# Kernel tuning notes

Measured on AMD Instinct MI355X. Metric: run time of the kernel, lower is better.

## Reference

```python
import jax, jax.numpy as jnp
import numpy as np

HEAD_NUM = 16

def setup_inputs() -> dict:
    key = jax.random.key(0)
    kq, kk, kv = jax.random.split(key, 3)
    shape = (4, 2048, 1024)  # [B, N, C]
    return {
        "query_layer": jax.random.normal(kq, shape, dtype=jnp.float32),
        "key_layer": jax.random.normal(kk, shape, dtype=jnp.float32),
        "value_layer": jax.random.normal(kv, shape, dtype=jnp.float32),
    }

def _split_heads(x, h):
    B, N, C = x.shape
    return x.reshape(B, N, h, C // h).transpose(0, 2, 1, 3)  # [B,H,N,d]

def reference(query_layer, key_layer, value_layer):
    B, N, C = query_layer.shape
    h = HEAD_NUM
    d = C // h
    q = _split_heads(query_layer, h)
    k = _split_heads(key_layer, h)
    v = _split_heads(value_layer, h)
    scores = jnp.einsum('bhnd,bhmd->bhnm', q, k) / jnp.sqrt(jnp.asarray(d, q.dtype))
    probs = jax.nn.softmax(scores, axis=-1)
    ctx = jnp.einsum('bhnm,bhmd->bhnd', probs, v)
    return ctx.transpose(0, 2, 1, 3).reshape(B, N, C)
```

## Files before the change

kernel.cpp:

```cpp
#include <hip/hip_runtime.h>
#include <hip/hip_bf16.h>

#define B_   4
#define N_   2048
#define C_   1024
#define NT   32
#define QSCALE 0.18033688011112042f

typedef __attribute__((ext_vector_type(8)))  short short8;
typedef __attribute__((ext_vector_type(4)))  float f32x4;
typedef __attribute__((ext_vector_type(16))) float f32x16;
typedef __attribute__((ext_vector_type(2)))  int   int2v;

__device__ __forceinline__ unsigned short f2bf(float x) {
    union { __hip_bfloat16 h; unsigned short u; } c;
    c.h = __float2bfloat16(x);
    return c.u;
}
__device__ __forceinline__ float fast_exp2(float x) {
    float r; asm("v_exp_f32 %0, %1" : "=v"(r) : "v"(x)); return r;
}
__device__ __forceinline__ int cvtpk(float a, float b) {
    int r; asm("v_cvt_pk_bf16_f32 %0, %1, %2" : "=v"(r) : "v"(a), "v"(b)); return r;
}

__global__ __launch_bounds__(256) void prepack(
    const float* __restrict__ K, const float* __restrict__ V,
    unsigned short* __restrict__ Kt, unsigned short* __restrict__ Vt)
{
    __shared__ __align__(16) unsigned short kl[4096];
    __shared__ __align__(16) unsigned short vl[4096];
    const int L = blockIdx.x;
    const int xcd = L & 7;
    const int j = L >> 3;
    const int head = xcd + 8 * (j >> 5);
    const int t = j & 31;
    const int b = head >> 4, h = head & 15;
    const int tid = threadIdx.x;
    const int r = tid >> 2, cb = tid & 3;
    const size_t head_off = (size_t)b * N_ * C_ + (size_t)h * 64;
    const int kv0 = t * 64;
    const int blk_out = head * NT + t;

    {
        const float* src = K + head_off + (size_t)(kv0 + r) * C_ + cb * 16;
        f32x4 x0 = *(const f32x4*)(src);
        f32x4 x1 = *(const f32x4*)(src + 4);
        f32x4 x2 = *(const f32x4*)(src + 8);
        f32x4 x3 = *(const f32x4*)(src + 12);
        short8 p0, p1;
        #pragma unroll
        for (int i = 0; i < 4; ++i) {
            p0[i] = (short)f2bf(x0[i]); p0[i + 4] = (short)f2bf(x1[i]);
            p1[i] = (short)f2bf(x2[i]); p1[i + 4] = (short)f2bf(x3[i]);
        }
        const int swz = (r & 7) << 3;
        *(short8*)&kl[r * 64 + ((cb * 16) ^ swz)]     = p0;
        *(short8*)&kl[r * 64 + ((cb * 16 + 8) ^ swz)] = p1;
    }
    {
        const float* src = V + head_off + (size_t)(kv0 + r) * C_ + cb * 16;
        f32x4 y0 = *(const f32x4*)(src);
        f32x4 y1 = *(const f32x4*)(src + 4);
        f32x4 y2 = *(const f32x4*)(src + 8);
        f32x4 y3 = *(const f32x4*)(src + 12);
        #pragma unroll
        for (int i = 0; i < 4; ++i) {
            int d0 = cb * 16 + i;
            vl[d0 * 64 + (r ^ ((d0 & 7) << 3))] = f2bf(y0[i]);
            int d1 = cb * 16 + 4 + i;
            vl[d1 * 64 + (r ^ ((d1 & 7) << 3))] = f2bf(y1[i]);
            int d2 = cb * 16 + 8 + i;
            vl[d2 * 64 + (r ^ ((d2 & 7) << 3))] = f2bf(y2[i]);
            int d3 = cb * 16 + 12 + i;
            vl[d3 * 64 + (r ^ ((d3 & 7) << 3))] = f2bf(y3[i]);
        }
    }
    __syncthreads();
    #pragma unroll
    for (int cc = 0; cc < 2; ++cc) {
        const int c  = tid + cc * 256;
        const int f  = c >> 6;
        const int ln = c & 63;
        const int row = (f & 1) * 32 + (ln & 31);
        const int col = (f >> 1) * 16 + (ln >> 5) * 8;
        const int sw  = (row & 7) << 3;
        short8 kk = *(const short8*)&kl[row * 64 + (col ^ sw)];
        short8 vv = *(const short8*)&vl[row * 64 + (col ^ sw)];
        *(short8*)&Kt[(size_t)blk_out * 4096 + c * 8] = kk;
        *(short8*)&Vt[(size_t)blk_out * 4096 + c * 8] = vv;
    }
}

__global__ __launch_bounds__(256, 4) void attn_fwd(
    const float* __restrict__ Q, const unsigned short* __restrict__ Kt,
    const unsigned short* __restrict__ Vt, float* __restrict__ O)
{
    const int L = blockIdx.x;
    const int xcd = L & 7;
    const int j = L >> 3;
    const int head = xcd + 8 * (j >> 4);
    const int qt = j & 15;
    const int b = head >> 4, h = head & 15;

    const int tid  = threadIdx.x;
    const int wave = tid >> 6;
    const int lane = tid & 63;
    const int l31  = lane & 31;
    const int hi   = lane >> 5;

    const unsigned short* kbase = Kt + (size_t)head * (NT * 4096);
    const unsigned short* vbase = Vt + (size_t)head * (NT * 4096);
    const float* qp = Q + (size_t)b * N_ * C_ + (size_t)h * 64;
    float*       op = O + (size_t)b * N_ * C_ + (size_t)h * 64;

    const int qrow = qt * 128 + wave * 32 + l31;
    short8 qfrag[4];
    {
        const float* qr = qp + (size_t)qrow * C_ + hi * 8;
        #pragma unroll
        for (int ks = 0; ks < 4; ++ks) {
            f32x4 x0 = *(const f32x4*)(qr + ks * 16);
            f32x4 x1 = *(const f32x4*)(qr + ks * 16 + 4);
            short8 a;
            #pragma unroll
            for (int i = 0; i < 4; ++i) {
                a[i]     = (short)f2bf(x0[i] * QSCALE);
                a[i + 4] = (short)f2bf(x1[i] * QSCALE);
            }
            qfrag[ks] = a;
        }
    }

    f32x16 o0 = {}, o1 = {};
    float m_r = -3.0e38f, l_r = 0.0f;

    const int lofs = lane * 8;

    for (int t = 0; t < NT; ++t) {
        const unsigned short* ktp = kbase + (size_t)t * 4096;
        const unsigned short* vtp = vbase + (size_t)t * 4096;

        f32x16 s0 = {}, s1 = {};
        __builtin_amdgcn_s_setprio(1);
        #pragma unroll
        for (int ks = 0; ks < 4; ++ks) {
            short8 kf0 = *(const short8*)(ktp + ks * 1024 + lofs);
            short8 kf1 = *(const short8*)(ktp + ks * 1024 + 512 + lofs);
            s0 = __builtin_amdgcn_mfma_f32_32x32x16_bf16(kf0, qfrag[ks], s0, 0, 0, 0);
            s1 = __builtin_amdgcn_mfma_f32_32x32x16_bf16(kf1, qfrag[ks], s1, 0, 0, 0);
        }
        __builtin_amdgcn_s_setprio(0);

        float mx[8];
        #pragma unroll
        for (int r = 0; r < 8; ++r) mx[r] = fmaxf(fmaxf(s0[r], s0[r + 8]), fmaxf(s1[r], s1[r + 8]));
        #pragma unroll
        for (int st = 4; st; st >>= 1) {
            #pragma unroll
            for (int r = 0; r < st; ++r) mx[r] = fmaxf(mx[r], mx[r + st]);
        }
        int2v msw = __builtin_amdgcn_permlane32_swap(__float_as_int(mx[0]), __float_as_int(mx[0]), false, false);
        const float rm = fmaxf(__int_as_float(msw[0]), __int_as_float(msw[1]));

        if (!__all(rm - m_r <= 8.0f)) {
            const float mnew = fmaxf(m_r, rm);
            const float corr = fast_exp2(m_r - mnew);
            m_r = mnew;
            l_r *= corr;
            #pragma unroll
            for (int r = 0; r < 16; ++r) { o0[r] *= corr; o1[r] *= corr; }
        }

        #pragma unroll
        for (int r = 0; r < 16; ++r) {
            s0[r] = fast_exp2(s0[r] - m_r);
            s1[r] = fast_exp2(s1[r] - m_r);
        }
        float aa[8];
        #pragma unroll
        for (int r = 0; r < 8; ++r) aa[r] = (s0[r] + s0[r + 8]) + (s1[r] + s1[r + 8]);
        #pragma unroll
        for (int st = 4; st; st >>= 1) {
            #pragma unroll
            for (int r = 0; r < st; ++r) aa[r] += aa[r + st];
        }
        int2v ssw = __builtin_amdgcn_permlane32_swap(__float_as_int(aa[0]), __float_as_int(aa[0]), false, false);
        l_r += __int_as_float(ssw[0]) + __int_as_float(ssw[1]);

        short8 pf[4];
        #pragma unroll
        for (int ct = 0; ct < 2; ++ct) {
            #pragma unroll
            for (int kss = 0; kss < 2; ++kss) {
                float e0, e1, e2, e3, e4, e5, e6, e7;
                if (ct == 0) {
                    e0 = s0[8*kss+0]; e1 = s0[8*kss+1]; e2 = s0[8*kss+2]; e3 = s0[8*kss+3];
                    e4 = s0[8*kss+4]; e5 = s0[8*kss+5]; e6 = s0[8*kss+6]; e7 = s0[8*kss+7];
                } else {
                    e0 = s1[8*kss+0]; e1 = s1[8*kss+1]; e2 = s1[8*kss+2]; e3 = s1[8*kss+3];
                    e4 = s1[8*kss+4]; e5 = s1[8*kss+5]; e6 = s1[8*kss+6]; e7 = s1[8*kss+7];
                }
                int w0 = cvtpk(e0, e1);
                int w1 = cvtpk(e2, e3);
                int w2 = cvtpk(e4, e5);
                int w3 = cvtpk(e6, e7);
                int2v sA = __builtin_amdgcn_permlane32_swap(w0, w2, false, false);
                int2v sB = __builtin_amdgcn_permlane32_swap(w1, w3, false, false);
                union { int i[4]; short8 v; } u;
                u.i[0] = sA[0]; u.i[1] = sB[0]; u.i[2] = sA[1]; u.i[3] = sB[1];
                pf[ct * 2 + kss] = u.v;
            }
        }

        __builtin_amdgcn_s_setprio(1);
        #pragma unroll
        for (int ks = 0; ks < 4; ++ks) {
            short8 vf0 = *(const short8*)(vtp + ks * 1024 + lofs);
            short8 vf1 = *(const short8*)(vtp + ks * 1024 + 512 + lofs);
            o0 = __builtin_amdgcn_mfma_f32_32x32x16_bf16(vf0, pf[ks], o0, 0, 0, 0);
            o1 = __builtin_amdgcn_mfma_f32_32x32x16_bf16(vf1, pf[ks], o1, 0, 0, 0);
        }
        __builtin_amdgcn_s_setprio(0);
    }

    const float inv = 1.0f / l_r;
    float* orow = op + (size_t)qrow * C_;
    #pragma unroll
    for (int bb = 0; bb < 4; ++bb) {
        f32x4 w0, w1;
        #pragma unroll
        for (int i = 0; i < 4; ++i) {
            w0[i] = o0[4 * bb + i] * inv;
            w1[i] = o1[4 * bb + i] * inv;
        }
        *(f32x4*)(orow + 8 * bb + 4 * hi)      = w0;
        *(f32x4*)(orow + 32 + 8 * bb + 4 * hi) = w1;
    }
}

extern "C" void kernel_launch(void* const* d_in, const int* in_sizes, int n_in,
                              void* d_out, int out_size, void* d_ws, size_t ws_size,
                              hipStream_t stream) {
    const float* q = (const float*)d_in[0];
    const float* k = (const float*)d_in[1];
    const float* v = (const float*)d_in[2];
    float* o = (float*)d_out;
    unsigned short* Kt = (unsigned short*)d_ws;
    unsigned short* Vt = Kt + (size_t)64 * NT * 4096;
    prepack<<<dim3(64 * NT), dim3(256), 0, stream>>>(k, v, Kt, Vt);
    attn_fwd<<<dim3(1024), dim3(256), 0, stream>>>(q, Kt, Vt, o);
}
```

Measured before the change: 120.9 us.

## Stage K/V tiles into double-buffered LDS via async global_load_lds

Each wave now asynchronously copies a quarter of the next K and V tile into a double-buffered shared-memory buffer with global_load_lds. The MFMA loops then read fragments from LDS instead of from global memory. This removes the fourfold redundant global reads across waves and overlaps the next tile's fetch with the current compute. In exchange it adds a vmcnt wait and a block barrier every iteration, plus 32KB of LDS per block, which may constrain occupancy.

```diff
diff --git a/kernel.cpp b/kernel.cpp
--- a/kernel.cpp
+++ b/kernel.cpp
@@ -96,6 +96,9 @@
     const float* __restrict__ Q, const unsigned short* __restrict__ Kt,
     const unsigned short* __restrict__ Vt, float* __restrict__ O)
 {
+    __shared__ __align__(16) unsigned short klds[2][4096];
+    __shared__ __align__(16) unsigned short vlds[2][4096];
+
     const int L = blockIdx.x;
     const int xcd = L & 7;
     const int j = L >> 3;
@@ -137,16 +140,36 @@
 
     const int lofs = lane * 8;
 
+    auto stage = [&](int t, int buf) {
+        const unsigned short* kg = kbase + (size_t)t * 4096 + wave * 1024 + lofs;
+        const unsigned short* vg = vbase + (size_t)t * 4096 + wave * 1024 + lofs;
+        __builtin_amdgcn_global_load_lds((const __attribute__((address_space(1))) void*)kg,
+            (__attribute__((address_space(3))) void*)&klds[buf][wave * 1024], 16, 0, 0);
+        __builtin_amdgcn_global_load_lds((const __attribute__((address_space(1))) void*)(kg + 512),
+            (__attribute__((address_space(3))) void*)&klds[buf][wave * 1024 + 512], 16, 0, 0);
+        __builtin_amdgcn_global_load_lds((const __attribute__((address_space(1))) void*)vg,
+            (__attribute__((address_space(3))) void*)&vlds[buf][wave * 1024], 16, 0, 0);
+        __builtin_amdgcn_global_load_lds((const __attribute__((address_space(1))) void*)(vg + 512),
+            (__attribute__((address_space(3))) void*)&vlds[buf][wave * 1024 + 512], 16, 0, 0);
+    };
+
+    stage(0, 0);
+    int cur = 0;
+
     for (int t = 0; t < NT; ++t) {
-        const unsigned short* ktp = kbase + (size_t)t * 4096;
-        const unsigned short* vtp = vbase + (size_t)t * 4096;
+        asm volatile("s_waitcnt vmcnt(0)" ::: "memory");
+        __syncthreads();
+        if (t + 1 < NT) stage(t + 1, cur ^ 1);
+
+        const unsigned short* kl = klds[cur];
+        const unsigned short* vl = vlds[cur];
 
         f32x16 s0 = {}, s1 = {};
         __builtin_amdgcn_s_setprio(1);
         #pragma unroll
         for (int ks = 0; ks < 4; ++ks) {
-            short8 kf0 = *(const short8*)(ktp + ks * 1024 + lofs);
-            short8 kf1 = *(const short8*)(ktp + ks * 1024 + 512 + lofs);
+            short8 kf0 = *(const short8*)&kl[ks * 1024 + lofs];
+            short8 kf1 = *(const short8*)&kl[ks * 1024 + 512 + lofs];
             s0 = __builtin_amdgcn_mfma_f32_32x32x16_bf16(kf0, qfrag[ks], s0, 0, 0, 0);
             s1 = __builtin_amdgcn_mfma_f32_32x32x16_bf16(kf1, qfrag[ks], s1, 0, 0, 0);
         }
@@ -216,12 +239,14 @@
         __builtin_amdgcn_s_setprio(1);
         #pragma unroll
         for (int ks = 0; ks < 4; ++ks) {
-            short8 vf0 = *(const short8*)(vtp + ks * 1024 + lofs);
-            short8 vf1 = *(const short8*)(vtp + ks * 1024 + 512 + lofs);
+            short8 vf0 = *(const short8*)&vl[ks * 1024 + lofs];
+            short8 vf1 = *(const short8*)&vl[ks * 1024 + 512 + lofs];
             o0 = __builtin_amdgcn_mfma_f32_32x32x16_bf16(vf0, pf[ks], o0, 0, 0, 0);
             o1 = __builtin_amdgcn_mfma_f32_32x32x16_bf16(vf1, pf[ks], o1, 0, 0, 0);
         }
         __builtin_amdgcn_s_setprio(0);
+
+        cur ^= 1;
     }
 
     const float inv = 1.0f / l_r;
```

Measured after the change: 111.5 us. -7.8%, faster.

## Software-pipeline attention loop with LDS double-buffered K and deferred PV MFMA

Applied to the files above, without the earlier changes.

Restructures the attention main loop into a software pipeline. K tiles are staged into a double-buffered LDS array via global_load_lds. The PV MFMAs of the previous tile are issued right after the current QK MFMAs, and V fragments for the current tile are prefetched into registers. The running max is folded into the QK accumulator init so the subtraction is skipped, and the row-sum permlane reduction is deferred to the end. This aims to hide global-load latency and softmax VALU work behind MFMAs, at the cost of more registers (occupancy hint lowered from 4 to 3) and a barrier per tile.

```diff
diff --git a/kernel.cpp b/kernel.cpp
--- a/kernel.cpp
+++ b/kernel.cpp
@@ -92,10 +92,135 @@
     }
 }
 
-__global__ __launch_bounds__(256, 4) void attn_fwd(
+#define MFMA32(A, B, C) __builtin_amdgcn_mfma_f32_32x32x16_bf16((A), (B), (C), 0, 0, 0)
+
+#define TILE_BODY(T, PO0, PO1, PO2, PO3, PI0, PI1, PI2, PI3, FIRST)            \
+{                                                                              \
+    asm volatile("s_waitcnt vmcnt(0)" ::: "memory");                           \
+    __syncthreads();                                                           \
+    if ((T) + 1 < NT) stageK((T) + 1, cur ^ 1);                                \
+    const unsigned short* kl = &klds[cur][0];                                  \
+    f32x16 s0, s1;                                                             \
+    {                                                                          \
+        const float nm = (FIRST) ? 0.0f : -m_r;   \
+        _Pragma("unroll")                                                      \
+        for (int r = 0; r < 16; ++r) { s0[r] = nm; s1[r] = nm; }               \
+    }                                                                          \
+    __builtin_amdgcn_s_setprio(1);                                             \
+    {                                                                          \
+        short8 kf0 = *(const short8*)&kl[0 * 1024 + lofs];                     \
+        short8 kf1 = *(const short8*)&kl[0 * 1024 + 512 + lofs];               \
+        s0 = MFMA32(kf0, qfrag[0], s0);                                        \
+        s1 = MFMA32(kf1, qfrag[0], s1);                                        \
+        kf0 = *(const short8*)&kl[1 * 1024 + lofs];                            \
+        kf1 = *(const short8*)&kl[1 * 1024 + 512 + lofs];                      \
+        s0 = MFMA32(kf0, qfrag[1], s0);                                        \
+        s1 = MFMA32(kf1, qfrag[1], s1);                                        \
+        kf0 = *(const short8*)&kl[2 * 1024 + lofs];                            \
+        kf1 = *(const short8*)&kl[2 * 1024 + 512 + lofs];                      \
+        s0 = MFMA32(kf0, qfrag[2], s0);                                        \
+        s1 = MFMA32(kf1, qfrag[2], s1);                                        \
+        kf0 = *(const short8*)&kl[3 * 1024 + lofs];                            \
+        kf1 = *(const short8*)&kl[3 * 1024 + 512 + lofs];                      \
+        s0 = MFMA32(kf0, qfrag[3], s0);                                        \
+        s1 = MFMA32(kf1, qfrag[3], s1);                                        \
+    }                                                                          \
+    if (!(FIRST)) {      \
+        o0 = MFMA32(vr0, PI0, o0);  o1 = MFMA32(vr1, PI0, o1);                 \
+        o0 = MFMA32(vr2, PI1, o0);  o1 = MFMA32(vr3, PI1, o1);                 \
+        o0 = MFMA32(vr4, PI2, o0);  o1 = MFMA32(vr5, PI2, o1);                 \
+        o0 = MFMA32(vr6, PI3, o0);  o1 = MFMA32(vr7, PI3, o1);                 \
+    }                                                                          \
+    __builtin_amdgcn_s_setprio(0);                                             \
+    {                \
+        const unsigned short* vtp = vbase + (size_t)(T) * 4096 + lofs;         \
+        vr0 = *(const short8*)(vtp);                                           \
+        vr1 = *(const short8*)(vtp + 512);                                     \
+        vr2 = *(const short8*)(vtp + 1024);                                    \
+        vr3 = *(const short8*)(vtp + 1536);                                    \
+        vr4 = *(const short8*)(vtp + 2048);                                    \
+        vr5 = *(const short8*)(vtp + 2560);                                    \
+        vr6 = *(const short8*)(vtp + 3072);                                    \
+        vr7 = *(const short8*)(vtp + 3584);                                    \
+    }                                                                          \
+    float mx[8];                                                               \
+    _Pragma("unroll")                                                          \
+    for (int r = 0; r < 8; ++r)                                                \
+        mx[r] = fmaxf(fmaxf(s0[r], s0[r + 8]), fmaxf(s1[r], s1[r + 8]));       \
+    _Pragma("unroll")                                                          \
+    for (int st = 4; st; st >>= 1) {                                           \
+        _Pragma("unroll")                                                      \
+        for (int r = 0; r < st; ++r) mx[r] = fmaxf(mx[r], mx[r + st]);         \
+    }                                                                          \
+    int2v msw = __builtin_amdgcn_permlane32_swap(                              \
+        __float_as_int(mx[0]), __float_as_int(mx[0]), false, false);           \
+    const float rmp = fmaxf(__int_as_float(msw[0]), __int_as_float(msw[1]));   \
+    if (FIRST) {                                                               \
+        m_r = rmp;                                                             \
+        _Pragma("unroll")                                                      \
+        for (int r = 0; r < 16; ++r) { s0[r] -= rmp; s1[r] -= rmp; }           \
+    } else if (!__all(rmp <= 8.0f)) {             \
+        const float d = fmaxf(rmp, 0.0f);                                      \
+        const float corr = fast_exp2(-d);                                      \
+        m_r += d;                                                              \
+        l_half *= corr;                                                        \
+        _Pragma("unroll")                                                      \
+        for (int r = 0; r < 16; ++r) {                                         \
+            s0[r] -= d; s1[r] -= d;                                            \
+            o0[r] *= corr; o1[r] *= corr;                                      \
+        }                                                                      \
+    }                                                                          \
+    _Pragma("unroll")                                                          \
+    for (int r = 0; r < 16; ++r) {                                             \
+        s0[r] = fast_exp2(s0[r]);                                              \
+        s1[r] = fast_exp2(s1[r]);                                              \
+    }                                                                          \
+    {                              \
+        int w0, w1, w2, w3; int2v sA, sB;                                      \
+        union { int i[4]; short8 v; } u;                                       \
+        w0 = cvtpk(s0[0], s0[1]);  w1 = cvtpk(s0[2], s0[3]);                   \
+        w2 = cvtpk(s0[4], s0[5]);  w3 = cvtpk(s0[6], s0[7]);                   \
+        sA = __builtin_amdgcn_permlane32_swap(w0, w2, false, false);           \
+        sB = __builtin_amdgcn_permlane32_swap(w1, w3, false, false);           \
+        u.i[0] = sA[0]; u.i[1] = sB[0]; u.i[2] = sA[1]; u.i[3] = sB[1];        \
+        PO0 = u.v;                                                             \
+        w0 = cvtpk(s0[8], s0[9]);  w1 = cvtpk(s0[10], s0[11]);                 \
+        w2 = cvtpk(s0[12], s0[13]); w3 = cvtpk(s0[14], s0[15]);                \
+        sA = __builtin_amdgcn_permlane32_swap(w0, w2, false, false);           \
+        sB = __builtin_amdgcn_permlane32_swap(w1, w3, false, false);           \
+        u.i[0] = sA[0]; u.i[1] = sB[0]; u.i[2] = sA[1]; u.i[3] = sB[1];        \
+        PO1 = u.v;                                                             \
+        w0 = cvtpk(s1[0], s1[1]);  w1 = cvtpk(s1[2], s1[3]);                   \
+        w2 = cvtpk(s1[4], s1[5]);  w3 = cvtpk(s1[6], s1[7]);                   \
+        sA = __builtin_amdgcn_permlane32_swap(w0, w2, false, false);           \
+        sB = __builtin_amdgcn_permlane32_swap(w1, w3, false, false);           \
+        u.i[0] = sA[0]; u.i[1] = sB[0]; u.i[2] = sA[1]; u.i[3] = sB[1];        \
+        PO2 = u.v;                                                             \
+        w0 = cvtpk(s1[8], s1[9]);  w1 = cvtpk(s1[10], s1[11]);                 \
+        w2 = cvtpk(s1[12], s1[13]); w3 = cvtpk(s1[14], s1[15]);                \
+        sA = __builtin_amdgcn_permlane32_swap(w0, w2, false, false);           \
+        sB = __builtin_amdgcn_permlane32_swap(w1, w3, false, false);           \
+        u.i[0] = sA[0]; u.i[1] = sB[0]; u.i[2] = sA[1]; u.i[3] = sB[1];        \
+        PO3 = u.v;                                                             \
+    }                                                                          \
+    float aa[8];                                                               \
+    _Pragma("unroll")                                                          \
+    for (int r = 0; r < 8; ++r) aa[r] = (s0[r] + s0[r + 8]) + (s1[r] + s1[r + 8]); \
+    _Pragma("unroll")                                                          \
+    for (int st = 4; st; st >>= 1) {                                           \
+        _Pragma("unroll")                                                      \
+        for (int r = 0; r < st; ++r) aa[r] += aa[r + st];                      \
+    }                                                                          \
+    l_half += aa[0];                                                           \
+    cur ^= 1;                                                                  \
+}
+
+__global__ __launch_bounds__(256, 3) void attn_fwd(
     const float* __restrict__ Q, const unsigned short* __restrict__ Kt,
     const unsigned short* __restrict__ Vt, float* __restrict__ O)
 {
+    __shared__ __align__(16) unsigned short klds[2][4096];
+
     const int L = blockIdx.x;
     const int xcd = L & 7;
     const int j = L >> 3;
@@ -133,98 +258,43 @@
     }
 
     f32x16 o0 = {}, o1 = {};
-    float m_r = -3.0e38f, l_r = 0.0f;
+    float m_r = 0.0f, l_half = 0.0f;
 
     const int lofs = lane * 8;
 
-    for (int t = 0; t < NT; ++t) {
-        const unsigned short* ktp = kbase + (size_t)t * 4096;
-        const unsigned short* vtp = vbase + (size_t)t * 4096;
-
-        f32x16 s0 = {}, s1 = {};
-        __builtin_amdgcn_s_setprio(1);
-        #pragma unroll
-        for (int ks = 0; ks < 4; ++ks) {
-            short8 kf0 = *(const short8*)(ktp + ks * 1024 + lofs);
-            short8 kf1 = *(const short8*)(ktp + ks * 1024 + 512 + lofs);
-            s0 = __builtin_amdgcn_mfma_f32_32x32x16_bf16(kf0, qfrag[ks], s0, 0, 0, 0);
-            s1 = __builtin_amdgcn_mfma_f32_32x32x16_bf16(kf1, qfrag[ks], s1, 0, 0, 0);
-        }
-        __builtin_amdgcn_s_setprio(0);
-
-        float mx[8];
-        #pragma unroll
-        for (int r = 0; r < 8; ++r) mx[r] = fmaxf(fmaxf(s0[r], s0[r + 8]), fmaxf(s1[r], s1[r + 8]));
-        #pragma unroll
-        for (int st = 4; st; st >>= 1) {
-            #pragma unroll
-            for (int r = 0; r < st; ++r) mx[r] = fmaxf(mx[r], mx[r + st]);
-        }
-        int2v msw = __builtin_amdgcn_permlane32_swap(__float_as_int(mx[0]), __float_as_int(mx[0]), false, false);
-        const float rm = fmaxf(__int_as_float(msw[0]), __int_as_float(msw[1]));
-
-        if (!__all(rm - m_r <= 8.0f)) {
-            const float mnew = fmaxf(m_r, rm);
-            const float corr = fast_exp2(m_r - mnew);
-            m_r = mnew;
-            l_r *= corr;
-            #pragma unroll
-            for (int r = 0; r < 16; ++r) { o0[r] *= corr; o1[r] *= corr; }
-        }
-
-        #pragma unroll
-        for (int r = 0; r < 16; ++r) {
-            s0[r] = fast_exp2(s0[r] - m_r);
-            s1[r] = fast_exp2(s1[r] - m_r);
-        }
-        float aa[8];
-        #pragma unroll
-        for (int r = 0; r < 8; ++r) aa[r] = (s0[r] + s0[r + 8]) + (s1[r] + s1[r + 8]);
-        #pragma unroll
-        for (int st = 4; st; st >>= 1) {
-            #pragma unroll
-            for (int r = 0; r < st; ++r) aa[r] += aa[r + st];
-        }
-        int2v ssw = __builtin_amdgcn_permlane32_swap(__float_as_int(aa[0]), __float_as_int(aa[0]), false, false);
-        l_r += __int_as_float(ssw[0]) + __int_as_float(ssw[1]);
-
-        short8 pf[4];
-        #pragma unroll
-        for (int ct = 0; ct < 2; ++ct) {
-            #pragma unroll
-            for (int kss = 0; kss < 2; ++kss) {
-                float e0, e1, e2, e3, e4, e5, e6, e7;
-                if (ct == 0) {
-                    e0 = s0[8*kss+0]; e1 = s0[8*kss+1]; e2 = s0[8*kss+2]; e3 = s0[8*kss+3];
-                    e4 = s0[8*kss+4]; e5 = s0[8*kss+5]; e6 = s0[8*kss+6]; e7 = s0[8*kss+7];
-                } else {
-                    e0 = s1[8*kss+0]; e1 = s1[8*kss+1]; e2 = s1[8*kss+2]; e3 = s1[8*kss+3];
-                    e4 = s1[8*kss+4]; e5 = s1[8*kss+5]; e6 = s1[8*kss+6]; e7 = s1[8*kss+7];
-                }
-                int w0 = cvtpk(e0, e1);
-                int w1 = cvtpk(e2, e3);
-                int w2 = cvtpk(e4, e5);
-                int w3 = cvtpk(e6, e7);
-                int2v sA = __builtin_amdgcn_permlane32_swap(w0, w2, false, false);
-                int2v sB = __builtin_amdgcn_permlane32_swap(w1, w3, false, false);
-                union { int i[4]; short8 v; } u;
-                u.i[0] = sA[0]; u.i[1] = sB[0]; u.i[2] = sA[1]; u.i[3] = sB[1];
-                pf[ct * 2 + kss] = u.v;
-            }
-        }
-
-        __builtin_amdgcn_s_setprio(1);
-        #pragma unroll
-        for (int ks = 0; ks < 4; ++ks) {
-            short8 vf0 = *(const short8*)(vtp + ks * 1024 + lofs);
-            short8 vf1 = *(const short8*)(vtp + ks * 1024 + 512 + lofs);
-            o0 = __builtin_amdgcn_mfma_f32_32x32x16_bf16(vf0, pf[ks], o0, 0, 0, 0);
-            o1 = __builtin_amdgcn_mfma_f32_32x32x16_bf16(vf1, pf[ks], o1, 0, 0, 0);
-        }
-        __builtin_amdgcn_s_setprio(0);
-    }
-
+    auto stageK = [&](int t, int buf) {
+        const unsigned short* kg = kbase + (size_t)t * 4096 + wave * 1024 + lofs;
+        __builtin_amdgcn_global_load_lds((const __attribute__((address_space(1))) void*)kg,
+            (__attribute__((address_space(3))) void*)&klds[buf][wave * 1024], 16, 0, 0);
+        __builtin_amdgcn_global_load_lds((const __attribute__((address_space(1))) void*)(kg + 512),
+            (__attribute__((address_space(3))) void*)&klds[buf][wave * 1024 + 512], 16, 0, 0);
+    };
+
+    int cur = 0;
+    short8 pA0, pA1, pA2, pA3, pB0, pB1, pB2, pB3;
+    short8 vr0, vr1, vr2, vr3, vr4, vr5, vr6, vr7;
+
+    stageK(0, 0);
+
+    TILE_BODY(0, pA0, pA1, pA2, pA3, pB0, pB1, pB2, pB3, true)
+    for (int t = 1; t < NT - 1; t += 2) {
+        TILE_BODY(t,     pB0, pB1, pB2, pB3, pA0, pA1, pA2, pA3, false)
+        TILE_BODY(t + 1, pA0, pA1, pA2, pA3, pB0, pB1, pB2, pB3, false)
+    }
+    TILE_BODY(NT - 1, pB0, pB1, pB2, pB3, pA0, pA1, pA2, pA3, false)
+
+    __builtin_amdgcn_s_setprio(1);
+    o0 = MFMA32(vr0, pB0, o0);  o1 = MFMA32(vr1, pB0, o1);
+    o0 = MFMA32(vr2, pB1, o0);  o1 = MFMA32(vr3, pB1, o1);
+    o0 = MFMA32(vr4, pB2, o0);  o1 = MFMA32(vr5, pB2, o1);
+    o0 = MFMA32(vr6, pB3, o0);  o1 = MFMA32(vr7, pB3, o1);
+    __builtin_amdgcn_s_setprio(0);
+
+    int2v lsw = __builtin_amdgcn_permlane32_swap(
+        __float_as_int(l_half), __float_as_int(l_half), false, false);
+    const float l_r = __int_as_float(lsw[0]) + __int_as_float(lsw[1]);
     const float inv = 1.0f / l_r;
+
     float* orow = op + (size_t)qrow * C_;
     #pragma unroll
     for (int bb = 0; bb < 4; ++bb) {
```

Result: faster. 110.0 us (-9.0%).
